# Kernel optimization log

Hardware: AMD Instinct MI355X
Metric: run time of the kernel (lower is better)

The kernel has to match this reference:

```python
import jax, jax.numpy as jnp
import numpy as np

N, Q, E, D = 100000, 128, 500000, 32
D4 = 4 * D
RATIO_UPDATE = 0.2
NEG_SLOPE = 0.01  # LeakyReLU default


def setup_inputs() -> dict:
    key = jax.random.key(0)
    ks = jax.random.split(key, 16)
    return {
        "visited_node_score": jax.random.uniform(ks[0], (N,), jnp.float32),
        "node_repr": jax.random.normal(ks[1], (N, D), jnp.float32),
        "eg0": jnp.sort(jax.random.randint(ks[2], (E,), 0, Q)),
        "src0": jax.random.randint(ks[3], (E,), 0, N),
        "dst0": jax.random.randint(ks[4], (E,), 0, N),
        "rel0": jax.random.normal(ks[5], (E, D), jnp.float32),
        "eg1": jnp.sort(jax.random.randint(ks[6], (E,), 0, Q)),
        "src1": jax.random.randint(ks[7], (E,), 0, N),
        "dst1": jax.random.randint(ks[8], (E,), 0, N),
        "rel1": jax.random.normal(ks[9], (E, D), jnp.float32),
        "query_src_emb": jax.random.normal(ks[10], (Q, D), jnp.float32),
        "query_rel_emb": jax.random.normal(ks[11], (Q, D), jnp.float32),
        "Wq": jax.random.normal(ks[12], (D4, D4), jnp.float32) * np.sqrt(2.0 / D4).astype(np.float32),
        "Wk": jax.random.normal(ks[13], (D4, D4), jnp.float32) * np.sqrt(2.0 / D4).astype(np.float32),
        "Wlin": jax.random.normal(ks[14], (D, D), jnp.float32) * np.sqrt(2.0 / (2 * D)).astype(np.float32),
        "blin": jnp.zeros((D,), jnp.float32),
        "max_edges": 500,
    }


def segment_softmax(logits, seg, num_segments):
    # softmax within groups of identical seg id (source node index)
    m = jax.ops.segment_max(logits, seg, num_segments=num_segments)
    ex = jnp.exp(logits - m[seg])
    s = jax.ops.segment_sum(ex, seg, num_segments=num_segments)
    return ex / s[seg]


def segment_topk_mask(values, seg, k):
    # keep mask for per-segment top-k (seg must be sorted); stable -> first occurrence on ties
    n = values.shape[0]
    order = jnp.lexsort((-values, seg))  # primary: seg, secondary: descending value
    seg_sorted = seg[order]
    idx = jnp.arange(n)
    is_start = jnp.concatenate([jnp.array([True]), seg_sorted[1:] != seg_sorted[:-1]])
    seg_start = jax.lax.cummax(jnp.where(is_start, idx, 0))
    rank_sorted = idx - seg_start  # rank within segment, 0 = largest
    rank = jnp.zeros((n,), jnp.int32).at[order].set(rank_sorted.astype(jnp.int32))
    return rank < k


def reference(visited_node_score, node_repr, eg0, src0, dst0, rel0,
              eg1, src1, dst1, rel1, query_src_emb, query_rel_emb,
              Wq, Wk, Wlin, blin, max_edges):
    def att_logits(repr_, src, dst, eg, rel):
        q = query_src_emb[eg]
        r = query_rel_emb[eg]
        left = jnp.concatenate([repr_[src], rel, q, r], axis=-1)   # [E, 4D]
        right = jnp.concatenate([repr_[dst], rel, q, r], axis=-1)  # [E, 4D]
        return jnp.sum((left @ Wq.T) * (right @ Wk.T), axis=-1)    # [E]

    num_nodes = node_repr.shape[0]

    # ---- last layer: attention + segmented top-k pruning ----
    logits1 = att_logits(node_repr, src1, dst1, eg1, rel1)
    w1 = segment_softmax(logits1, src1, num_nodes)           # softmax over out-edges of each src node
    src_score = visited_node_score[src1]
    target_score = w1 * src_score
    keep = segment_topk_mask(target_score, eg1, max_edges)   # top-k per eg_idx
    w1p = jnp.where(keep, w1, 0.0)

    # node score aggregation == 'sum': score[n] = sum_{kept e: dst=n} w * src_score
    updated_node_score = jax.ops.segment_sum(w1p * src_score, dst1, num_segments=num_nodes)

    # representation update along pruned edges (linear_act=False)
    agg = jax.ops.segment_sum(w1p[:, None] * node_repr[src1], dst1, num_segments=num_nodes)
    repr_ = (1.0 - RATIO_UPDATE) * agg + RATIO_UPDATE * node_repr

    # ---- earlier layer(s), no pruning ----
    logits0 = att_logits(repr_, src0, dst0, eg0, rel0)
    w0 = segment_softmax(logits0, src0, num_nodes)
    agg0 = jax.ops.segment_sum(w0[:, None] * repr_[src0], dst0, num_segments=num_nodes)
    repr_ = (1.0 - RATIO_UPDATE) * agg0 + RATIO_UPDATE * repr_

    # bypass_forward: LeakyReLU(Linear(repr))
    h = repr_ @ Wlin.T + blin
    updated_repr = jnp.where(h >= 0, h, NEG_SLOPE * h)
    return updated_node_score, updated_repr
```

## Files before the change

### kernel.cpp

```cpp
#include <hip/hip_runtime.h>
#include <math.h>

#define DD 32
#define DD4 128
#define TPB 256
#define LDSCAP 6144
#define CANDCAP 2048

__device__ __forceinline__ unsigned long long dsort_key(double x) {
  unsigned long long b = (unsigned long long)__double_as_longlong(x);
  return (b & 0x8000000000000000ull) ? ~b : (b | 0x8000000000000000ull);
}
__device__ __forceinline__ double dunsort_key(unsigned long long k) {
  unsigned long long b = (k & 0x8000000000000000ull) ? (k ^ 0x8000000000000000ull) : ~k;
  return __longlong_as_double((long long)b);
}
__device__ __forceinline__ unsigned int fsort_key(float x) {
  unsigned int b = __float_as_uint(x);
  return (b & 0x80000000u) ? ~b : (b | 0x80000000u);
}
__device__ __forceinline__ float funsort_key(unsigned int k) {
  unsigned int b = (k & 0x80000000u) ? (k ^ 0x80000000u) : ~k;
  return __uint_as_float(b);
}

typedef float f32x4 __attribute__((ext_vector_type(4)));
__device__ __forceinline__ float4 nt_load4(const float* p) {
  f32x4 v = __builtin_nontemporal_load((const f32x4*)p);
  return make_float4(v.x, v.y, v.z, v.w);
}

__device__ __forceinline__ int block_iscan256(int x, int* wsum) {
  const int lane = threadIdx.x & 63, w = threadIdx.x >> 6;
#pragma unroll
  for (int o = 1; o < 64; o <<= 1) {
    int y = __shfl_up(x, o, 64);
    if (lane >= o) x += y;
  }
  if (lane == 63) wsum[w] = x;
  __syncthreads();
  int add = 0;
#pragma unroll
  for (int i = 0; i < 4; ++i) add += (i < w) ? wsum[i] : 0;
  __syncthreads();
  return x + add;
}

__global__ __launch_bounds__(TPB) void k_precompute_M(
    const float* __restrict__ Wq, const float* __restrict__ Wk,
    double* __restrict__ M64, float* __restrict__ M32) {
  int t = blockIdx.x * blockDim.x + threadIdx.x;
  int i = t >> 7, j = t & 127;
  double acc = 0.0;
  for (int k = 0; k < DD4; ++k)
    acc += (double)Wq[k * DD4 + i] * (double)Wk[k * DD4 + j];
  M64[i * DD4 + j] = acc;
  M32[i * DD4 + j] = (float)acc;
}

__global__ __launch_bounds__(TPB) void k_sym22(
    const double* __restrict__ M64, double* __restrict__ S64, float* __restrict__ S32) {
  int i = blockIdx.x * blockDim.x + threadIdx.x;
  int r = i >> 5, c = i & 31;
  double g  = M64[(32 + r) * DD4 + 32 + c];
  double gt = M64[(32 + c) * DD4 + 32 + r];
  double s = (c > r) ? (g + gt) : ((c == r) ? g : 0.0);
  S64[i] = s;
  S32[i] = (float)s;
}

__global__ __launch_bounds__(64) void k_per_query(
    const double* __restrict__ M64,
    const float* __restrict__ qemb, const float* __restrict__ remb,
    double* __restrict__ p64, double* __restrict__ pD64, double* __restrict__ c64,
    float* __restrict__ p32, float* __restrict__ pD32, float* __restrict__ c32) {
  int q = blockIdx.x;
  int l = threadIdx.x;
  __shared__ double qr[64];
  qr[l] = (l < DD) ? (double)qemb[q * DD + l] : (double)remb[q * DD + (l - DD)];
  __syncthreads();
  double a = 0.0;
  for (int j = 0; j < 64; ++j) a += M64[l * DD4 + 64 + j] * qr[j];
  double ct = 0.0;
  for (int j = 0; j < 64; ++j) ct += M64[(64 + j) * DD4 + l] * qr[j];
  if (l >= DD) a += ct;
  p64[q * 64 + l] = a;
  p32[q * 64 + l] = (float)a;
  if (l < DD) {
    pD64[q * DD + l] = ct;
    pD32[q * DD + l] = (float)ct;
  }
  double a3 = 0.0;
  for (int j = 0; j < 64; ++j) a3 += M64[(64 + l) * DD4 + 64 + j] * qr[j];
  a3 *= qr[l];
  for (int o = 32; o; o >>= 1) a3 += __shfl_xor(a3, o);
  if (l == 0) { c64[q] = a3; c32[q] = (float)a3; }
}

#define G_T(c) Mmat[(c) * DD4 + j]
#define G_U(c) Mmat[j * DD4 + 32 + (c)]
#define G_V(c) Mmat[(32 + (c)) * DD4 + j]

#define NP_TILE(GEXPR)                                                          \
  for (int tt = 0; tt < 4; ++tt) {                                              \
    T a0=(T)0,a1=(T)0,a2=(T)0,a3=(T)0,a4=(T)0,a5=(T)0,a6=(T)0,a7=(T)0;          \
    const int c0 = tt * 8;                                                      \
    _Pragma("unroll")                                                           \
    for (int j = 0; j < 32; ++j) {                                              \
      const T hj = hh[j];                                                       \
      a0 += (GEXPR(c0 + 0)) * hj; a1 += (GEXPR(c0 + 1)) * hj;                   \
      a2 += (GEXPR(c0 + 2)) * hj; a3 += (GEXPR(c0 + 3)) * hj;                   \
      a4 += (GEXPR(c0 + 4)) * hj; a5 += (GEXPR(c0 + 5)) * hj;                   \
      a6 += (GEXPR(c0 + 6)) * hj; a7 += (GEXPR(c0 + 7)) * hj;                   \
    }                                                                           \
    xq[tid * 9 + tt * 2]     = make_float4((float)a0,(float)a1,(float)a2,(float)a3); \
    xq[tid * 9 + tt * 2 + 1] = make_float4((float)a4,(float)a5,(float)a6,(float)a7); \
  }

#define NP_STORE(dst)                                                           \
  __syncthreads();                                                              \
  {                                                                             \
    float4* go = (float4*)(dst) + (size_t)nbase * 8;                            \
    _Pragma("unroll")                                                           \
    for (int k = 0; k < 8; ++k) {                                               \
      int f = k * TPB + tid;                                                    \
      if ((f >> 3) < nlim) go[f] = xq[(f >> 3) * 9 + (f & 7)];                  \
    }                                                                           \
  }                                                                             \
  __syncthreads();

template <typename T, bool MIX>
__global__ __launch_bounds__(TPB) void k_node_pre(
    const T* __restrict__ Mmat, const float* __restrict__ reprIn,
    const float* __restrict__ aggIn, float* __restrict__ reprOut,
    float* __restrict__ t, float* __restrict__ u, float* __restrict__ v, int N_) {
  __shared__ float xp[TPB * 36];
  float4* xq = (float4*)xp;
  const int tid = threadIdx.x;
  const int nbase = blockIdx.x * TPB;
  const int n = nbase + tid;
  const int nlim = min(TPB, N_ - nbase);
  const bool valid = tid < nlim;
  T hh[32];
  if (valid) {
    const float4* h4 = (const float4*)reprIn + (size_t)n * 8;
#pragma unroll
    for (int jq = 0; jq < 8; ++jq) {
      float4 x = h4[jq];
      if constexpr (MIX) {
        const float4 a = ((const float4*)aggIn)[(size_t)n * 8 + jq];
        x = make_float4(0.8f * a.x + 0.2f * x.x, 0.8f * a.y + 0.2f * x.y,
                        0.8f * a.z + 0.2f * x.z, 0.8f * a.w + 0.2f * x.w);
        xq[tid * 9 + jq] = x;
      }
      hh[4 * jq]     = (T)x.x; hh[4 * jq + 1] = (T)x.y;
      hh[4 * jq + 2] = (T)x.z; hh[4 * jq + 3] = (T)x.w;
    }
  } else {
#pragma unroll
    for (int j = 0; j < 32; ++j) hh[j] = (T)0;
  }
  if constexpr (MIX) {
    NP_STORE(reprOut)
  }
  NP_TILE(G_T)
  NP_STORE(t)
  NP_TILE(G_U)
  NP_STORE(u)
  NP_TILE(G_V)
  NP_STORE(v)
}

template <typename T>
__global__ __launch_bounds__(TPB) void k_quad(
    const T* __restrict__ Smat,
    const float* __restrict__ rel, const int* __restrict__ eg,
    const T* __restrict__ pq, const T* __restrict__ cq,
    T* __restrict__ quad, int E) {
  const int e = blockIdx.x * TPB + threadIdx.x;
  if (e >= E) return;
  const int q = eg[e];
  T rl[32];
  {
    const float* rbase = rel + (size_t)e * 32;
#pragma unroll
    for (int j = 0; j < 8; ++j) {
      float4 x = nt_load4(rbase + j * 4);
      rl[4 * j] = (T)x.x; rl[4 * j + 1] = (T)x.y;
      rl[4 * j + 2] = (T)x.z; rl[4 * j + 3] = (T)x.w;
    }
  }
  const T* prow = pq + (size_t)q * 64 + 32;
  T lin0 = (T)0, lin1 = (T)0;
#pragma unroll
  for (int i = 0; i < 32; i += 2) {
    lin0 += prow[i] * rl[i];
    lin1 += prow[i + 1] * rl[i + 1];
  }
  T a0 = cq[q] + lin0, a1 = lin1, a2 = (T)0, a3 = (T)0;
#pragma unroll
  for (int i = 0; i < 32; ++i) {
    T r0 = Smat[i * 32 + i] * rl[i];
    T r1 = (T)0;
#pragma unroll
    for (int j = i + 1; j < 32; ++j) {
      if ((j - i) & 1) r1 += Smat[i * 32 + j] * rl[j];
      else             r0 += Smat[i * 32 + j] * rl[j];
    }
    T rr = (r0 + r1) * rl[i];
    if ((i & 3) == 0) a0 += rr;
    else if ((i & 3) == 1) a1 += rr;
    else if ((i & 3) == 2) a2 += rr;
    else a3 += rr;
  }
  quad[e] = (a0 + a1) + (a2 + a3);
}

template <typename T>
__global__ __launch_bounds__(TPB) void k_edge_dots(
    const float* __restrict__ repr, const float* __restrict__ rel,
    const int* __restrict__ src, const int* __restrict__ dst, const int* __restrict__ eg,
    const float* __restrict__ tvec, const float* __restrict__ uvec, const float* __restrict__ vvec,
    const T* __restrict__ pq, const T* __restrict__ pDq, const T* __restrict__ quad,
    T* __restrict__ logits, void* __restrict__ mkey, int E) {
  const long long t = (long long)blockIdx.x * TPB + threadIdx.x;
  const int e = (int)(t >> 3), part = (int)(t & 7);
  if (e >= E) return;
  const int s = src[e], d = dst[e], q = eg[e];
  const float4 hs = ((const float4*)repr)[(size_t)s * 8 + part];
  const float4 td = ((const float4*)tvec)[(size_t)d * 8 + part];
  const float4 hd = ((const float4*)repr)[(size_t)d * 8 + part];
  const float4 rl = nt_load4(rel + ((size_t)e * 8 + part) * 4);
  const float4 us = ((const float4*)uvec)[(size_t)s * 8 + part];
  const float4 vd = ((const float4*)vvec)[(size_t)d * 8 + part];
  const T* p  = pq  + (size_t)q * 64 + part * 4;
  const T* pD = pDq + (size_t)q * DD + part * 4;
  T a = (T)hs.x * ((T)td.x + p[0]) + (T)hs.y * ((T)td.y + p[1]) +
        (T)hs.z * ((T)td.z + p[2]) + (T)hs.w * ((T)td.w + p[3]);
  a += (T)hd.x * pD[0] + (T)hd.y * pD[1] + (T)hd.z * pD[2] + (T)hd.w * pD[3];
  a += (T)rl.x * (T)(us.x + vd.x) + (T)rl.y * (T)(us.y + vd.y) +
       (T)rl.z * (T)(us.z + vd.z) + (T)rl.w * (T)(us.w + vd.w);
  a += __shfl_xor(a, 1);
  a += __shfl_xor(a, 2);
  a += __shfl_xor(a, 4);
  if (part == 0) {
    a += quad[e];
    logits[e] = a;
    if constexpr (sizeof(T) == 8) {
      atomicMax((unsigned long long*)mkey + s, dsort_key((double)a));
    } else {
      atomicMax((unsigned int*)mkey + s, fsort_key((float)a));
    }
  }
}

__global__ __launch_bounds__(TPB) void k_expsum64(
    double* __restrict__ io, const unsigned long long* __restrict__ mkey,
    const int* __restrict__ src, const int* __restrict__ eg,
    double* __restrict__ ssum, int* __restrict__ qoff, int E, int Q) {
  int e = blockIdx.x * blockDim.x + threadIdx.x;
  if (e >= E) return;
  int s = src[e];
  double ex = exp(io[e] - dunsort_key(mkey[s]));
  io[e] = ex;
  atomicAdd(&ssum[s], ex);
  int cur = eg[e];
  int prev = (e == 0) ? -1 : eg[e - 1];
  for (int v = prev + 1; v <= cur; ++v) qoff[v] = e;
  if (e == E - 1) {
    for (int v = cur + 1; v <= Q; ++v) qoff[v] = E;
  }
}
__global__ __launch_bounds__(TPB) void k_expsum32h(
    float* __restrict__ io, const unsigned int* __restrict__ mkey,
    const int* __restrict__ src, const int* __restrict__ dst,
    float* __restrict__ ssum, int* __restrict__ cnt, int E) {
  int e = blockIdx.x * blockDim.x + threadIdx.x;
  if (e >= E) return;
  int s = src[e];
  float ex = expf(io[e] - funsort_key(mkey[s]));
  io[e] = ex;
  atomicAdd(&ssum[s], ex);
  atomicAdd(&cnt[dst[e]], 1);
}

__global__ __launch_bounds__(TPB) void k_topk(
    const double* __restrict__ ex, const double* __restrict__ ssum,
    const int* __restrict__ src, const float* __restrict__ score,
    const int* __restrict__ qoff, const int* __restrict__ maxe,
    unsigned int* __restrict__ tkeyg, float* __restrict__ w1fg,
    float* __restrict__ w1p, int E) {
  __shared__ unsigned int keys[LDSCAP];
  __shared__ float wval[LDSCAP];
  __shared__ int hist[256];
  __shared__ unsigned short cand[CANDCAP];
  __shared__ int wsum[4];
  __shared__ int sh_cnt;
  __shared__ unsigned int sh_prefix;
  __shared__ int sh_need;
  const int q = blockIdx.x;
  const int s = qoff[q], e2 = qoff[q + 1];
  const int n = e2 - s;
  const int K = maxe[0];
  if (n <= K) {
    for (int i = s + threadIdx.x; i < e2; i += TPB) {
      int sv = src[i];
      w1p[i] = (float)(ex[i] / ssum[sv]);
    }
    return;
  }
  const bool useLds = (n <= LDSCAP);
  if (useLds) {
    for (int i = threadIdx.x; i < n; i += TPB) {
      int sv = src[s + i];
      float wf = (float)(ex[s + i] / ssum[sv]);
      wval[i] = wf;
      keys[i] = fsort_key(wf * score[sv]);
    }
  } else {
    for (int i = s + threadIdx.x; i < e2; i += TPB) {
      int sv = src[i];
      float wf = (float)(ex[i] / ssum[sv]);
      w1fg[i] = wf;
      tkeyg[i] = fsort_key(wf * score[sv]);
    }
  }
  hist[threadIdx.x] = 0;
  __syncthreads();
  for (int i = threadIdx.x; i < n; i += TPB) {
    unsigned int k = useLds ? keys[i] : tkeyg[s + i];
    atomicAdd(&hist[k >> 24], 1);
  }
  __syncthreads();
  int need = K;
  {
    int h = hist[255 - threadIdx.x];
    int incl = block_iscan256(h, wsum);
    int excl = incl - h;
    if (incl >= need && excl < need) {
      sh_prefix = (unsigned int)(255 - threadIdx.x) << 24;
      sh_need = need - excl;
    }
  }
  __syncthreads();
  unsigned int prefix = sh_prefix;
  need = sh_need;
  const int cnt0 = hist[prefix >> 24];
  const bool compact = useLds && (cnt0 <= CANDCAP);
  if (threadIdx.x == 0) sh_cnt = 0;
  __syncthreads();
  if (compact) {
    const unsigned int d0 = prefix >> 24;
    for (int i = threadIdx.x; i < n; i += TPB) {
      if ((keys[i] >> 24) == d0) {
        int p = atomicAdd(&sh_cnt, 1);
        cand[p] = (unsigned short)i;
      }
    }
  }
  __syncthreads();
  const int ncand = compact ? sh_cnt : 0;
  for (int pass = 1; pass < 4; ++pass) {
    const int shift = 24 - 8 * pass;
    const unsigned int himask = 0xFFFFFFFFu << (shift + 8);
    hist[threadIdx.x] = 0;
    __syncthreads();
    if (compact) {
      for (int ci = threadIdx.x; ci < ncand; ci += TPB) {
        unsigned int k = keys[cand[ci]];
        if ((k & himask) == prefix) atomicAdd(&hist[(k >> shift) & 255], 1);
      }
    } else {
      for (int i = threadIdx.x; i < n; i += TPB) {
        unsigned int k = useLds ? keys[i] : tkeyg[s + i];
        if ((k & himask) == prefix) atomicAdd(&hist[(k >> shift) & 255], 1);
      }
    }
    __syncthreads();
    int h = hist[255 - threadIdx.x];
    int incl = block_iscan256(h, wsum);
    int excl = incl - h;
    if (incl >= need && excl < need) {
      sh_prefix = prefix | ((unsigned int)(255 - threadIdx.x) << shift);
      sh_need = need - excl;
    }
    __syncthreads();
    prefix = sh_prefix;
    need = sh_need;
    __syncthreads();
  }
  const unsigned int kth = prefix;
  const int r = need;
  const int C = (n + TPB - 1) / TPB;
  const int b0 = min(threadIdx.x * C, n);
  const int b1 = min(b0 + C, n);
  int myt = 0;
  for (int i = b0; i < b1; ++i) {
    unsigned int k = useLds ? keys[i] : tkeyg[s + i];
    myt += (k == kth) ? 1 : 0;
  }
  int tincl = block_iscan256(myt, wsum);
  int tiepre = tincl - myt;
  for (int i = b0; i < b1; ++i) {
    unsigned int k = useLds ? keys[i] : tkeyg[s + i];
    float v = 0.f;
    if (k > kth) {
      v = useLds ? wval[i] : w1fg[s + i];
    } else if (k == kth) {
      if (tiepre < r) v = useLds ? wval[i] : w1fg[s + i];
      ++tiepre;
    }
    w1p[s + i] = v;
  }
}

__global__ __launch_bounds__(TPB) void k_apply1(
    const float* __restrict__ w1p, const int* __restrict__ src, const int* __restrict__ dst,
    const float* __restrict__ repr0, const float* __restrict__ score,
    float* __restrict__ agg, float* __restrict__ score_out, int E) {
  int t = blockIdx.x * blockDim.x + threadIdx.x;
  int e = t >> 3, part = t & 7;
  if (e >= E) return;
  float w = w1p[e];
  if (w == 0.f) return;
  int sv = src[e], dv = dst[e];
  const float4 rv = ((const float4*)repr0)[sv * 8 + part];
  float* ap = agg + (size_t)dv * DD + part * 4;
  atomicAdd(ap + 0, w * rv.x);
  atomicAdd(ap + 1, w * rv.y);
  atomicAdd(ap + 2, w * rv.z);
  atomicAdd(ap + 3, w * rv.w);
  if (part == 0) atomicAdd(score_out + dv, w * score[sv]);
}

#define SCHUNK 1024
__global__ __launch_bounds__(TPB) void k_scan1(
    const int* __restrict__ cnt, int* __restrict__ off, int* __restrict__ bsum, int N_) {
  __shared__ int sd[TPB];
  const int b = blockIdx.x, t = threadIdx.x;
  const int base = b * SCHUNK + t * 4;
  int v[4];
  int s4 = 0;
#pragma unroll
  for (int k = 0; k < 4; ++k) {
    v[k] = (base + k < N_) ? cnt[base + k] : 0;
    s4 += v[k];
  }
  sd[t] = s4;
  __syncthreads();
  for (int o = 1; o < TPB; o <<= 1) {
    int x = (t >= o) ? sd[t - o] : 0;
    __syncthreads();
    sd[t] += x;
    __syncthreads();
  }
  int excl = sd[t] - s4;
  if (t == TPB - 1) bsum[b] = sd[t];
  int run = excl;
#pragma unroll
  for (int k = 0; k < 4; ++k) {
    if (base + k < N_) { off[base + k] = run; run += v[k]; }
  }
}

__global__ __launch_bounds__(TPB) void k_scan2(
    int* __restrict__ bsum, int* __restrict__ off, int nblk, int N_, int E) {
  __shared__ int wsum[4];
  if (nblk <= TPB) {
    int t = threadIdx.x;
    int x = (t < nblk) ? bsum[t] : 0;
    int orig = x;
    const int lane = t & 63, w = t >> 6;
#pragma unroll
    for (int o = 1; o < 64; o <<= 1) {
      int y = __shfl_up(x, o, 64);
      if (lane >= o) x += y;
    }
    if (lane == 63) wsum[w] = x;
    __syncthreads();
    int add = 0;
#pragma unroll
    for (int i = 0; i < 4; ++i) add += (i < w) ? wsum[i] : 0;
    x += add;
    if (t < nblk) bsum[t] = x - orig;
    if (t == 0) off[N_] = E;
  } else {
    if (threadIdx.x != 0) return;
    int run = 0;
    for (int i = 0; i < nblk; ++i) { int tmp = bsum[i]; bsum[i] = run; run += tmp; }
    off[N_] = E;
  }
}

__global__ __launch_bounds__(TPB) void k_scan3(
    int* __restrict__ off, const int* __restrict__ bsum, int* __restrict__ cursor, int N_) {
  int i = blockIdx.x * blockDim.x + threadIdx.x;
  if (i >= N_) return;
  int v = off[i] + bsum[i >> 10];
  off[i] = v;
  cursor[i] = v;
}

__global__ __launch_bounds__(TPB) void k_scatter0(
    const float* __restrict__ ex, const float* __restrict__ ssum,
    const int* __restrict__ src, const int* __restrict__ dst,
    int* __restrict__ cursor, float2* __restrict__ pk, int E) {
  int e = blockIdx.x * blockDim.x + threadIdx.x;
  if (e >= E) return;
  int s = src[e];
  float w = ex[e] / ssum[s];
  int pos = atomicAdd(&cursor[dst[e]], 1);
  pk[pos] = make_float2(w, __int_as_float(s));
}

__global__ __launch_bounds__(TPB) void k_gather_mix(
    const float2* __restrict__ pk, const int* __restrict__ off,
    const float* __restrict__ repr1, float* __restrict__ mixbuf, int N_) {
  const int n = blockIdx.x * 8 + (threadIdx.x >> 5);
  const int c = threadIdx.x & 31;
  if (n >= N_) return;
  const float self = repr1[(size_t)n * DD + c];
  float acc = 0.f;
  const int j0 = off[n], j1 = off[n + 1];
  int j = j0;
  for (; j + 4 <= j1; j += 4) {
    const float2 p0 = pk[j], p1 = pk[j + 1], p2 = pk[j + 2], p3 = pk[j + 3];
    const float g0 = repr1[(size_t)__float_as_int(p0.y) * DD + c];
    const float g1 = repr1[(size_t)__float_as_int(p1.y) * DD + c];
    const float g2 = repr1[(size_t)__float_as_int(p2.y) * DD + c];
    const float g3 = repr1[(size_t)__float_as_int(p3.y) * DD + c];
    acc += p0.x * g0;
    acc += p1.x * g1;
    acc += p2.x * g2;
    acc += p3.x * g3;
  }
  for (; j < j1; ++j) {
    const float2 p = pk[j];
    acc += p.x * repr1[(size_t)__float_as_int(p.y) * DD + c];
  }
  mixbuf[(size_t)n * DD + c] = 0.8f * acc + 0.2f * self;
}

__global__ __launch_bounds__(TPB) void k_final_linear(
    const float* __restrict__ Wlin, const float* __restrict__ blin,
    const float* __restrict__ mixbuf, float* __restrict__ out_repr, int N_) {
  __shared__ float xp[TPB * 36];
  float4* xq = (float4*)xp;
  const int tid = threadIdx.x;
  const int nbase = blockIdx.x * TPB;
  const int n = nbase + tid;
  const int nlim = min(TPB, N_ - nbase);
  float m[32];
  if (tid < nlim) {
    const float4* h4 = (const float4*)mixbuf + (size_t)n * 8;
#pragma unroll
    for (int jq = 0; jq < 8; ++jq) {
      float4 x = h4[jq];
      m[4 * jq] = x.x; m[4 * jq + 1] = x.y; m[4 * jq + 2] = x.z; m[4 * jq + 3] = x.w;
    }
  } else {
#pragma unroll
    for (int j = 0; j < 32; ++j) m[j] = 0.f;
  }
  for (int tt = 0; tt < 4; ++tt) {
    const int c0 = tt * 8;
    float a0 = blin[c0 + 0], a1 = blin[c0 + 1], a2 = blin[c0 + 2], a3 = blin[c0 + 3];
    float a4 = blin[c0 + 4], a5 = blin[c0 + 5], a6 = blin[c0 + 6], a7 = blin[c0 + 7];
#pragma unroll
    for (int j = 0; j < 32; ++j) {
      const float hj = m[j];
      a0 += Wlin[(c0 + 0) * DD + j] * hj; a1 += Wlin[(c0 + 1) * DD + j] * hj;
      a2 += Wlin[(c0 + 2) * DD + j] * hj; a3 += Wlin[(c0 + 3) * DD + j] * hj;
      a4 += Wlin[(c0 + 4) * DD + j] * hj; a5 += Wlin[(c0 + 5) * DD + j] * hj;
      a6 += Wlin[(c0 + 6) * DD + j] * hj; a7 += Wlin[(c0 + 7) * DD + j] * hj;
    }
    a0 = (a0 >= 0.f) ? a0 : 0.01f * a0; a1 = (a1 >= 0.f) ? a1 : 0.01f * a1;
    a2 = (a2 >= 0.f) ? a2 : 0.01f * a2; a3 = (a3 >= 0.f) ? a3 : 0.01f * a3;
    a4 = (a4 >= 0.f) ? a4 : 0.01f * a4; a5 = (a5 >= 0.f) ? a5 : 0.01f * a5;
    a6 = (a6 >= 0.f) ? a6 : 0.01f * a6; a7 = (a7 >= 0.f) ? a7 : 0.01f * a7;
    xq[tid * 9 + tt * 2]     = make_float4(a0, a1, a2, a3);
    xq[tid * 9 + tt * 2 + 1] = make_float4(a4, a5, a6, a7);
  }
  NP_STORE(out_repr)
}

extern "C" void kernel_launch(void* const* d_in, const int* in_sizes, int n_in,
                              void* d_out, int out_size, void* d_ws, size_t ws_size,
                              hipStream_t stream) {
  (void)n_in; (void)out_size; (void)ws_size;
  const float* score = (const float*)d_in[0];
  const float* nrepr = (const float*)d_in[1];
  const int*   eg0   = (const int*)d_in[2];
  const int*   src0  = (const int*)d_in[3];
  const int*   dst0  = (const int*)d_in[4];
  const float* rel0  = (const float*)d_in[5];
  const int*   eg1   = (const int*)d_in[6];
  const int*   src1  = (const int*)d_in[7];
  const int*   dst1  = (const int*)d_in[8];
  const float* rel1  = (const float*)d_in[9];
  const float* qemb  = (const float*)d_in[10];
  const float* remb  = (const float*)d_in[11];
  const float* Wq    = (const float*)d_in[12];
  const float* Wk    = (const float*)d_in[13];
  const float* Wlin  = (const float*)d_in[14];
  const float* blin  = (const float*)d_in[15];
  const int*   maxe  = (const int*)d_in[16];

  const int N_ = in_sizes[0];
  const int E_ = in_sizes[2];
  const int Q_ = in_sizes[10] / DD;

  char* wsc = (char*)d_ws;
  size_t off = 0;
  auto alloc = [&](size_t bytes) -> void* {
    void* p = wsc + off;
    off += (bytes + 255) & ~(size_t)255;
    return p;
  };
  double* M64  = (double*)alloc((size_t)DD4 * DD4 * 8);
  float*  M32  = (float*)alloc((size_t)DD4 * DD4 * 4);
  double* S64  = (double*)alloc((size_t)DD * DD * 8);
  float*  S32  = (float*)alloc((size_t)DD * DD * 4);
  double* p64  = (double*)alloc((size_t)Q_ * 64 * 8);
  double* pD64 = (double*)alloc((size_t)Q_ * DD * 8);
  double* c64  = (double*)alloc((size_t)Q_ * 8);
  float*  p32  = (float*)alloc((size_t)Q_ * 64 * 4);
  float*  pD32 = (float*)alloc((size_t)Q_ * DD * 4);
  float*  c32  = (float*)alloc((size_t)Q_ * 4);
  int*    qoff = (int*)alloc((size_t)(Q_ + 2) * 4);
  double* lg1  = (double*)alloc((size_t)E_ * 8);
  double* qv64 = (double*)alloc((size_t)E_ * 8);
  float*  w1f  = (float*)alloc((size_t)E_ * 4);
  unsigned int* tkey = (unsigned int*)alloc((size_t)E_ * 4);
  float*  w1p  = (float*)alloc((size_t)E_ * 4);
  float*  lg0  = (float*)alloc((size_t)E_ * 4);
  float*  repr1 = (float*)alloc((size_t)N_ * DD * 4);
  float*  tvec = (float*)alloc((size_t)N_ * DD * 4);
  float*  uvec = (float*)alloc((size_t)N_ * DD * 4);
  float*  vvec = (float*)alloc((size_t)N_ * DD * 4);
  size_t zstart = off;
  unsigned long long* mkey1 = (unsigned long long*)alloc((size_t)N_ * 8);
  double* s1   = (double*)alloc((size_t)N_ * 8);
  float*  agg  = (float*)alloc((size_t)N_ * DD * 4);
  unsigned int* mkey0 = (unsigned int*)alloc((size_t)N_ * 4);
  float*  s0   = (float*)alloc((size_t)N_ * 4);
  size_t zlen = off - zstart;

  float* qv32 = (float*)qv64;

  int* cnt    = (int*)tvec;
  int* offcsr = (int*)tvec + N_;
  int* cursor = (int*)tvec + 2 * (size_t)N_ + 64;
  int* bsum   = (int*)tvec + 3 * (size_t)N_ + 128;
  float2* pk  = (float2*)uvec;
  float* mixbuf = vvec;

  float* out_score = (float*)d_out;
  float* out_repr  = out_score + N_;

  hipMemsetAsync(wsc + zstart, 0, zlen, stream);
  hipMemsetAsync(d_out, 0, (size_t)N_ * 4, stream);

  k_precompute_M<<<(DD4 * DD4) / TPB, TPB, 0, stream>>>(Wq, Wk, M64, M32);
  k_sym22<<<4, TPB, 0, stream>>>(M64, S64, S32);
  k_per_query<<<Q_, 64, 0, stream>>>(M64, qemb, remb, p64, pD64, c64, p32, pD32, c32);

  const int ngrid = (N_ + TPB - 1) / TPB;
  const int egrid = (E_ + TPB - 1) / TPB;
  const int dgrid = (int)(((size_t)E_ * 8 + TPB - 1) / TPB);

  k_node_pre<double, false><<<ngrid, TPB, 0, stream>>>(M64, nrepr, nullptr, nullptr,
                                                       tvec, uvec, vvec, N_);
  k_quad<double><<<egrid, TPB, 0, stream>>>(S64, rel1, eg1, p64, c64, qv64, E_);
  k_edge_dots<double><<<dgrid, TPB, 0, stream>>>(nrepr, rel1, src1, dst1, eg1,
                                                 tvec, uvec, vvec, p64, pD64, qv64,
                                                 lg1, (void*)mkey1, E_);
  k_expsum64<<<egrid, TPB, 0, stream>>>(lg1, mkey1, src1, eg1, s1, qoff, E_, Q_);
  k_topk<<<Q_, TPB, 0, stream>>>(lg1, s1, src1, score, qoff, maxe, tkey, w1f, w1p, E_);

  k_apply1<<<dgrid, TPB, 0, stream>>>(w1p, src1, dst1, nrepr, score, agg, out_score, E_);

  k_node_pre<float, true><<<ngrid, TPB, 0, stream>>>(M32, nrepr, agg, repr1,
                                                     tvec, uvec, vvec, N_);
  k_quad<float><<<egrid, TPB, 0, stream>>>(S32, rel0, eg0, p32, c32, qv32, E_);
  k_edge_dots<float><<<dgrid, TPB, 0, stream>>>(repr1, rel0, src0, dst0, eg0,
                                                tvec, uvec, vvec, p32, pD32, qv32,
                                                lg0, (void*)mkey0, E_);

  hipMemsetAsync(cnt, 0, (size_t)N_ * 4, stream);
  k_expsum32h<<<egrid, TPB, 0, stream>>>(lg0, mkey0, src0, dst0, s0, cnt, E_);
  const int nblk = (N_ + SCHUNK - 1) / SCHUNK;
  k_scan1<<<nblk, TPB, 0, stream>>>(cnt, offcsr, bsum, N_);
  k_scan2<<<1, TPB, 0, stream>>>(bsum, offcsr, nblk, N_, E_);
  k_scan3<<<ngrid, TPB, 0, stream>>>(offcsr, bsum, cursor, N_);
  k_scatter0<<<egrid, TPB, 0, stream>>>(lg0, s0, src0, dst0, cursor, pk, E_);
  k_gather_mix<<<(N_ + 7) / 8, TPB, 0, stream>>>(pk, offcsr, repr1, mixbuf, N_);
  k_final_linear<<<ngrid, TPB, 0, stream>>>(Wlin, blin, mixbuf, out_repr, N_);
}
```

Measured before the change: 640.5 us.

## Move softmax weight and top-k key computation into edge-parallel kernel

Adds an edge-parallel kernel that computes normalized softmax weights, target-score sort keys and per-query offsets over all edges. The per-query top-k kernel, which runs only Q blocks, then reads precomputed keys instead of doing divisions and gathers itself, which spreads that work across the whole GPU. It also replaces nontemporal loads of the relation vectors with ordinary float4 loads. The cost is one extra kernel launch and an extra global write and read of the weight and key arrays.

```diff
diff --git a/kernel.cpp b/kernel.cpp
--- a/kernel.cpp
+++ b/kernel.cpp
@@ -22,12 +22,6 @@
 __device__ __forceinline__ float funsort_key(unsigned int k) {
   unsigned int b = (k & 0x80000000u) ? (k ^ 0x80000000u) : ~k;
   return __uint_as_float(b);
-}
-
-typedef float f32x4 __attribute__((ext_vector_type(4)));
-__device__ __forceinline__ float4 nt_load4(const float* p) {
-  f32x4 v = __builtin_nontemporal_load((const f32x4*)p);
-  return make_float4(v.x, v.y, v.z, v.w);
 }
 
 __device__ __forceinline__ int block_iscan256(int x, int* wsum) {
@@ -182,10 +176,10 @@
   const int q = eg[e];
   T rl[32];
   {
-    const float* rbase = rel + (size_t)e * 32;
+    const float4* r4 = (const float4*)rel + (size_t)e * 8;
 #pragma unroll
     for (int j = 0; j < 8; ++j) {
-      float4 x = nt_load4(rbase + j * 4);
+      float4 x = r4[j];
       rl[4 * j] = (T)x.x; rl[4 * j + 1] = (T)x.y;
       rl[4 * j + 2] = (T)x.z; rl[4 * j + 3] = (T)x.w;
     }
@@ -230,7 +224,7 @@
   const float4 hs = ((const float4*)repr)[(size_t)s * 8 + part];
   const float4 td = ((const float4*)tvec)[(size_t)d * 8 + part];
   const float4 hd = ((const float4*)repr)[(size_t)d * 8 + part];
-  const float4 rl = nt_load4(rel + ((size_t)e * 8 + part) * 4);
+  const float4 rl = ((const float4*)rel)[(size_t)e * 8 + part];
   const float4 us = ((const float4*)uvec)[(size_t)s * 8 + part];
   const float4 vd = ((const float4*)vvec)[(size_t)d * 8 + part];
   const T* p  = pq  + (size_t)q * 64 + part * 4;
@@ -256,20 +250,13 @@
 
 __global__ __launch_bounds__(TPB) void k_expsum64(
     double* __restrict__ io, const unsigned long long* __restrict__ mkey,
-    const int* __restrict__ src, const int* __restrict__ eg,
-    double* __restrict__ ssum, int* __restrict__ qoff, int E, int Q) {
+    const int* __restrict__ src, double* __restrict__ ssum, int E) {
   int e = blockIdx.x * blockDim.x + threadIdx.x;
   if (e >= E) return;
   int s = src[e];
   double ex = exp(io[e] - dunsort_key(mkey[s]));
   io[e] = ex;
   atomicAdd(&ssum[s], ex);
-  int cur = eg[e];
-  int prev = (e == 0) ? -1 : eg[e - 1];
-  for (int v = prev + 1; v <= cur; ++v) qoff[v] = e;
-  if (e == E - 1) {
-    for (int v = cur + 1; v <= Q; ++v) qoff[v] = E;
-  }
 }
 __global__ __launch_bounds__(TPB) void k_expsum32h(
     float* __restrict__ io, const unsigned int* __restrict__ mkey,
@@ -284,14 +271,32 @@
   atomicAdd(&cnt[dst[e]], 1);
 }
 
-__global__ __launch_bounds__(TPB) void k_topk(
+__global__ __launch_bounds__(TPB) void k_weights_target(
     const double* __restrict__ ex, const double* __restrict__ ssum,
     const int* __restrict__ src, const float* __restrict__ score,
+    const int* __restrict__ eg, int* __restrict__ qoff,
+    float* __restrict__ w1f, unsigned int* __restrict__ tkey, int E, int Q) {
+  int e = blockIdx.x * blockDim.x + threadIdx.x;
+  if (e >= E) return;
+  int s = src[e];
+  double w = ex[e] / ssum[s];
+  float wf = (float)w;
+  w1f[e] = wf;
+  float tgt = wf * score[s];
+  tkey[e] = fsort_key(tgt);
+  int cur = eg[e];
+  int prev = (e == 0) ? -1 : eg[e - 1];
+  for (int v = prev + 1; v <= cur; ++v) qoff[v] = e;
+  if (e == E - 1) {
+    for (int v = cur + 1; v <= Q; ++v) qoff[v] = E;
+  }
+}
+
+__global__ __launch_bounds__(TPB) void k_topk(
+    const unsigned int* __restrict__ tkey, const float* __restrict__ w1f,
     const int* __restrict__ qoff, const int* __restrict__ maxe,
-    unsigned int* __restrict__ tkeyg, float* __restrict__ w1fg,
     float* __restrict__ w1p, int E) {
   __shared__ unsigned int keys[LDSCAP];
-  __shared__ float wval[LDSCAP];
   __shared__ int hist[256];
   __shared__ unsigned short cand[CANDCAP];
   __shared__ int wsum[4];
@@ -303,32 +308,17 @@
   const int n = e2 - s;
   const int K = maxe[0];
   if (n <= K) {
-    for (int i = s + threadIdx.x; i < e2; i += TPB) {
-      int sv = src[i];
-      w1p[i] = (float)(ex[i] / ssum[sv]);
-    }
+    for (int i = s + threadIdx.x; i < e2; i += TPB) w1p[i] = w1f[i];
     return;
   }
   const bool useLds = (n <= LDSCAP);
   if (useLds) {
-    for (int i = threadIdx.x; i < n; i += TPB) {
-      int sv = src[s + i];
-      float wf = (float)(ex[s + i] / ssum[sv]);
-      wval[i] = wf;
-      keys[i] = fsort_key(wf * score[sv]);
-    }
-  } else {
-    for (int i = s + threadIdx.x; i < e2; i += TPB) {
-      int sv = src[i];
-      float wf = (float)(ex[i] / ssum[sv]);
-      w1fg[i] = wf;
-      tkeyg[i] = fsort_key(wf * score[sv]);
-    }
+    for (int i = threadIdx.x; i < n; i += TPB) keys[i] = tkey[s + i];
   }
   hist[threadIdx.x] = 0;
   __syncthreads();
   for (int i = threadIdx.x; i < n; i += TPB) {
-    unsigned int k = useLds ? keys[i] : tkeyg[s + i];
+    unsigned int k = useLds ? keys[i] : tkey[s + i];
     atomicAdd(&hist[k >> 24], 1);
   }
   __syncthreads();
@@ -372,7 +362,7 @@
       }
     } else {
       for (int i = threadIdx.x; i < n; i += TPB) {
-        unsigned int k = useLds ? keys[i] : tkeyg[s + i];
+        unsigned int k = useLds ? keys[i] : tkey[s + i];
         if ((k & himask) == prefix) atomicAdd(&hist[(k >> shift) & 255], 1);
       }
     }
@@ -396,18 +386,18 @@
   const int b1 = min(b0 + C, n);
   int myt = 0;
   for (int i = b0; i < b1; ++i) {
-    unsigned int k = useLds ? keys[i] : tkeyg[s + i];
+    unsigned int k = useLds ? keys[i] : tkey[s + i];
     myt += (k == kth) ? 1 : 0;
   }
   int tincl = block_iscan256(myt, wsum);
   int tiepre = tincl - myt;
   for (int i = b0; i < b1; ++i) {
-    unsigned int k = useLds ? keys[i] : tkeyg[s + i];
+    unsigned int k = useLds ? keys[i] : tkey[s + i];
     float v = 0.f;
     if (k > kth) {
-      v = useLds ? wval[i] : w1fg[s + i];
+      v = w1f[s + i];
     } else if (k == kth) {
-      if (tiepre < r) v = useLds ? wval[i] : w1fg[s + i];
+      if (tiepre < r) v = w1f[s + i];
       ++tiepre;
     }
     w1p[s + i] = v;
@@ -675,8 +665,10 @@
   k_edge_dots<double><<<dgrid, TPB, 0, stream>>>(nrepr, rel1, src1, dst1, eg1,
                                                  tvec, uvec, vvec, p64, pD64, qv64,
                                                  lg1, (void*)mkey1, E_);
-  k_expsum64<<<egrid, TPB, 0, stream>>>(lg1, mkey1, src1, eg1, s1, qoff, E_, Q_);
-  k_topk<<<Q_, TPB, 0, stream>>>(lg1, s1, src1, score, qoff, maxe, tkey, w1f, w1p, E_);
+  k_expsum64<<<egrid, TPB, 0, stream>>>(lg1, mkey1, src1, s1, E_);
+  k_weights_target<<<egrid, TPB, 0, stream>>>(lg1, s1, src1, score, eg1, qoff,
+                                              w1f, tkey, E_, Q_);
+  k_topk<<<Q_, TPB, 0, stream>>>(tkey, w1f, qoff, maxe, w1p, E_);
 
   k_apply1<<<dgrid, TPB, 0, stream>>>(w1p, src1, dst1, nrepr, score, agg, out_score, E_);
 
```

Measured after the change: 623.6 us. 2.6% less time.
